# Kernel tuning notes

Hardware: AMD Instinct MI355X
Metric: run time of the kernel (lower is better)

The kernel has to match this reference:

```python
import jax, jax.numpy as jnp
import numpy as np

B, CIN, COUT, N, R, K = 8, 64, 64, 4096, 32, 3
LEAK = 0.2
BN_EPS = 1e-5
GN_EPS = 1e-5


def _voxelize(features, coords, r):
    # features: [B,C,N], coords: [B,3,N] -> grid [B,C,r,r,r], norm_coords [B,3,N]
    norm = coords - coords.mean(axis=2, keepdims=True)
    scale = jnp.max(jnp.linalg.norm(norm, axis=1, keepdims=True), axis=2, keepdims=True) * 2.0
    norm = norm / scale + 0.5
    norm = jnp.clip(norm * r, 0.0, r - 1.0)
    vox = jnp.round(norm).astype(jnp.int32)            # [B,3,N]
    idx = vox[:, 0] * (r * r) + vox[:, 1] * r + vox[:, 2]  # [B,N]
    b, c, n = features.shape
    r3 = r * r * r
    seg = (jnp.arange(b, dtype=jnp.int32)[:, None] * r3 + idx).reshape(-1)  # [B*N]
    feat = features.transpose(0, 2, 1).reshape(b * n, c)  # [B*N,C]
    sums = jax.ops.segment_sum(feat, seg, num_segments=b * r3)             # [B*r3,C]
    cnt = jax.ops.segment_sum(jnp.ones((b * n,), feat.dtype), seg, num_segments=b * r3)
    mean = sums / jnp.maximum(cnt, 1.0)[:, None]
    grid = mean.reshape(b, r3, c).transpose(0, 2, 1).reshape(b, c, r, r, r)
    return grid, norm


def _devoxelize(grid, norm_coords, r):
    # grid: [B,C,r,r,r], norm_coords: [B,3,N] in [0, r-1] -> [B,C,N]
    b, c = grid.shape[:2]
    flat = grid.reshape(b, c, r * r * r)
    cpos = jnp.clip(norm_coords, 0.0, r - 1.0)
    f = jnp.floor(cpos)
    d = cpos - f                                        # [B,3,N] frac
    i0 = f.astype(jnp.int32)
    i1 = jnp.minimum(i0 + 1, r - 1)
    out = jnp.zeros((b, c, norm_coords.shape[2]), grid.dtype)
    for dx in (0, 1):
        wx = d[:, 0] if dx else (1.0 - d[:, 0])
        ix = i1[:, 0] if dx else i0[:, 0]
        for dy in (0, 1):
            wy = d[:, 1] if dy else (1.0 - d[:, 1])
            iy = i1[:, 1] if dy else i0[:, 1]
            for dz in (0, 1):
                wz = d[:, 2] if dz else (1.0 - d[:, 2])
                iz = i1[:, 2] if dz else i0[:, 2]
                idx = ix * (r * r) + iy * r + iz        # [B,N]
                g = jnp.take_along_axis(flat, idx[:, None, :], axis=2)  # [B,C,N]
                out = out + (wx * wy * wz)[:, None, :] * g
    return out


def _conv3d(x, w, b):
    y = jax.lax.conv_general_dilated(x, w, window_strides=(1, 1, 1), padding='SAME',
                                     dimension_numbers=('NCDHW', 'OIDHW', 'NCDHW'))
    return y + b[None, :, None, None, None]


def _bn3d(x, g, bta, m, v):
    inv = g / jnp.sqrt(v + BN_EPS)
    return x * inv[None, :, None, None, None] + (bta - m * inv)[None, :, None, None, None]


def _leaky(x):
    return jnp.where(x >= 0, x, LEAK * x)


def _point_mlp(x, w, b, gg, gb):
    # Conv1d 1x1 + GroupNorm(8) + Swish; x: [B,Cin,N]
    y = jnp.einsum('oc,bcn->bon', w, x) + b[None, :, None]
    bb, cc, nn = y.shape
    yg = y.reshape(bb, 8, cc // 8, nn)
    mu = yg.mean(axis=(2, 3), keepdims=True)
    var = yg.var(axis=(2, 3), keepdims=True)
    yn = ((yg - mu) / jnp.sqrt(var + GN_EPS)).reshape(bb, cc, nn)
    yn = yn * gg[None, :, None] + gb[None, :, None]
    return yn * jax.nn.sigmoid(yn)  # Swish


def setup_inputs() -> dict:
    key = jax.random.key(0)
    ks = jax.random.split(key, 12)
    s3 = 1.0 / np.sqrt(CIN * K ** 3)
    s3b = 1.0 / np.sqrt(COUT * K ** 3)
    return {
        'features': jax.random.normal(ks[0], (B, CIN, N), jnp.float32),
        'coords': jax.random.normal(ks[1], (B, 3, N), jnp.float32),
        'temb': jax.random.normal(ks[2], (B, 64), jnp.float32),
        'conv1_w': jax.random.normal(ks[3], (COUT, CIN, K, K, K), jnp.float32) * s3,
        'conv1_b': jnp.zeros((COUT,), jnp.float32),
        'bn1_g': jnp.ones((COUT,), jnp.float32),
        'bn1_b': jnp.zeros((COUT,), jnp.float32),
        'bn1_m': jnp.zeros((COUT,), jnp.float32),
        'bn1_v': jnp.ones((COUT,), jnp.float32),
        'conv2_w': jax.random.normal(ks[4], (COUT, COUT, K, K, K), jnp.float32) * s3b,
        'conv2_b': jnp.zeros((COUT,), jnp.float32),
        'bn2_g': jnp.ones((COUT,), jnp.float32),
        'bn2_b': jnp.zeros((COUT,), jnp.float32),
        'bn2_m': jnp.zeros((COUT,), jnp.float32),
        'bn2_v': jnp.ones((COUT,), jnp.float32),
        'pf_w': jax.random.normal(ks[5], (COUT, CIN), jnp.float32) / np.sqrt(CIN),
        'pf_b': jnp.zeros((COUT,), jnp.float32),
        'gn_g': jnp.ones((COUT,), jnp.float32),
        'gn_b': jnp.zeros((COUT,), jnp.float32),
    }


def reference(features, coords, temb,
              conv1_w, conv1_b, bn1_g, bn1_b, bn1_m, bn1_v,
              conv2_w, conv2_b, bn2_g, bn2_b, bn2_m, bn2_v,
              pf_w, pf_b, gn_g, gn_b):
    grid, norm_coords = _voxelize(features, jax.lax.stop_gradient(coords), R)
    h = _leaky(_bn3d(_conv3d(grid, conv1_w, conv1_b), bn1_g, bn1_b, bn1_m, bn1_v))
    # dropout: identity in eval mode
    h = _leaky(_bn3d(_conv3d(h, conv2_w, conv2_b), bn2_g, bn2_b, bn2_m, bn2_v))
    vox_pts = _devoxelize(h, norm_coords, R)           # [B,COUT,N]
    fused = vox_pts + _point_mlp(features, pf_w, pf_b, gn_g, gn_b)
    return fused, coords, temb
```

## Files before the change

### kernel.cpp

```cpp
#include <hip/hip_runtime.h>
#include <hip/hip_bf16.h>
#include <math.h>

#define BB 8
#define CH 64
#define NP 4096
#define RG 32
#define R3 32768
#define LEAK 0.2f
#define BNEPS 1e-5f
#define GNEPS 1e-5f
#define SS3 602

typedef short short8 __attribute__((ext_vector_type(8)));
typedef float float4_ __attribute__((ext_vector_type(4)));

__device__ __forceinline__ short f2bf(float f){
  unsigned u = __float_as_uint(f);
  u += 0x7FFF + ((u>>16)&1);
  return (short)(u>>16);
}
__device__ __forceinline__ float bf2f(short s){
  unsigned u = ((unsigned)(unsigned short)s)<<16;
  return __uint_as_float(u);
}

__global__ void k_voxstats(const float* __restrict__ coords, float* __restrict__ ms){
  int b = blockIdx.x;
  __shared__ float red[256];
  float mean[3];
  for(int d=0; d<3; d++){
    float s=0.f;
    for(int i=threadIdx.x; i<NP; i+=256) s += coords[(b*3+d)*NP+i];
    red[threadIdx.x]=s; __syncthreads();
    for(int o=128;o>0;o>>=1){ if(threadIdx.x<o) red[threadIdx.x]+=red[threadIdx.x+o]; __syncthreads(); }
    mean[d]=red[0]/(float)NP; __syncthreads();
  }
  float mx=0.f;
  for(int i=threadIdx.x; i<NP; i+=256){
    float x=coords[(b*3+0)*NP+i]-mean[0];
    float y=coords[(b*3+1)*NP+i]-mean[1];
    float z=coords[(b*3+2)*NP+i]-mean[2];
    mx=fmaxf(mx, sqrtf(x*x+y*y+z*z));
  }
  red[threadIdx.x]=mx; __syncthreads();
  for(int o=128;o>0;o>>=1){ if(threadIdx.x<o) red[threadIdx.x]=fmaxf(red[threadIdx.x],red[threadIdx.x+o]); __syncthreads(); }
  if(threadIdx.x==0){
    ms[b*4+0]=mean[0]; ms[b*4+1]=mean[1]; ms[b*4+2]=mean[2];
    ms[b*4+3]=red[0]*2.0f;
  }
}

__global__ void k_assignzero(const float* __restrict__ coords, const float* __restrict__ ms,
                             float* __restrict__ nc, int* __restrict__ vi,
                             float* __restrict__ gsum){
  int bid=blockIdx.x;
  int blk=(bid&7)*1024 + (bid>>3);
  int wid = (blk*256+threadIdx.x)>>6;
  int lane = threadIdx.x&63;
  if(wid>=BB*NP) return;
  int b=wid>>12, n=wid&4095;
  float scale=ms[b*4+3];
  float v[3]; int vox[3];
  #pragma unroll
  for(int d=0; d<3; d++){
    float c=coords[(b*3+d)*NP+n] - ms[b*4+d];
    float vv=(c/scale + 0.5f)*32.0f;
    vv=fminf(fmaxf(vv,0.0f),31.0f);
    v[d]=vv;
    vox[d]=(int)rintf(vv);
  }
  int idx=vox[0]*1024+vox[1]*32+vox[2];
  if(lane<3) nc[(b*3+lane)*NP+n]=v[lane];
  if(lane==0) vi[wid]=idx;
  gsum[((size_t)b*R3+idx)*CH + lane]=0.f;
}

__global__ __launch_bounds__(256,2) void k_scatter(
    const float* __restrict__ feat, const int* __restrict__ vi,
    float* __restrict__ gsum, float* __restrict__ cnt){
  __shared__ float ft[64][65];
  int tid=threadIdx.x;
  int bid=blockIdx.x;
  int blk=(bid&7)*64 + (bid>>3);
  int b=blk>>6, n0=(blk&63)*64;
  for(int e=tid;e<4096;e+=256){
    int c=e>>6, nl=e&63;
    ft[nl][c]=feat[(size_t)(b*CH+c)*NP + n0+nl];
  }
  __syncthreads();
  int lane=tid&63, wv=tid>>6;
  for(int p=wv;p<64;p+=4){
    int idx=vi[(b<<12)+n0+p];
    atomicAdd(gsum + ((size_t)b*R3+idx)*CH + lane, ft[p][lane]);
    if(lane==0) atomicAdd(&cnt[b*R3+idx], 1.0f);
  }
}

__global__ void k_gridmean(const float* __restrict__ gsum, const float* __restrict__ cnt,
                           short* __restrict__ gbf){
  int bid=blockIdx.x;
  int blk=(bid&7)*1024 + (bid>>3);
  int t=blk*256+threadIdx.x;
  if(t>=BB*R3*8) return;
  int v=t>>3, q=t&7;
  float c=cnt[v];
  short8 o={0,0,0,0,0,0,0,0};
  if(c!=0.f){
    float inv=1.0f/c;
    const float* sp=gsum + (size_t)v*CH + q*8;
    #pragma unroll
    for(int j=0;j<8;j++) o[j]=f2bf(sp[j]*inv);
  }
  ((short8*)gbf)[(size_t)v*8+q]=o;
}

__global__ void k_wt3x2(const float* __restrict__ wa, const float* __restrict__ wb,
                        short* __restrict__ oa, short* __restrict__ ob){
  int t=blockIdx.x*256+threadIdx.x;
  if(t>=2*CH*CH*27) return;
  const float* w = (t<CH*CH*27)? wa : wb;
  short* o = (t<CH*CH*27)? oa : ob;
  int tt = (t<CH*CH*27)? t : t-CH*CH*27;
  int frag=tt>>9, l=(tt>>3)&63, j=tt&7;
  int tap=frag>>3, hh=(frag>>2)&1, nf=frag&3;
  int oc=nf*16+(l&15);
  int ci=hh*32+(l>>4)*8+j;
  o[tt]=f2bf(w[oc*1728 + ci*27 + tap]);
}

#define CONV_TAP(AF, BW) \
  _Pragma("unroll") for(int ks=0;ks<2;ks++) \
    _Pragma("unroll") for(int mf=0;mf<4;mf++) \
      _Pragma("unroll") for(int nf=0;nf<4;nf++) \
        acc[mf][nf]=__builtin_amdgcn_mfma_f32_16x16x32_bf16(AF[ks*4+mf],BW[ks*4+nf],acc[mf][nf],0,0,0);

__global__ __launch_bounds__(256,2) void k_conv_mfma(
    const short* __restrict__ gin, short* __restrict__ gout,
    const short* __restrict__ wt3, const float* __restrict__ bias,
    const float* __restrict__ bg, const float* __restrict__ bb,
    const float* __restrict__ bm, const float* __restrict__ bv){
  extern __shared__ __align__(16) short in_s[];
  int tid=threadIdx.x;
  int bid=blockIdx.x;
  int blk=(bid&7)*128 + (bid>>3);
  int b=blk>>7; int rem=blk&127;
  int zt=rem>>4, yt=(rem>>2)&3, xt=rem&3;
  int z0=zt*4, y0=yt*8, x0=xt*8;
  const short* gbase = gin + (size_t)b*R3*CH;

  int lane=tid&63, zl=tid>>6;
  int r15=lane&15, g=lane>>4;
  int ix=r15&7, iy=r15>>3;

  float4_ acc[4][4];
  #pragma unroll
  for(int mf=0;mf<4;mf++)
    #pragma unroll
    for(int nf=0;nf<4;nf++) acc[mf][nf]=(float4_){0.f,0.f,0.f,0.f};

  short8* s8=(short8*)in_s;

  for(int it=0; it<19; it++){
    int e=tid+it*256;
    if(e<4800){
      int ss=e>>3, cb=e&7;
      int z=ss/100, r2=ss-z*100, y=r2/10, x=r2-y*10;
      int gz=z0-1+z, gy=y0-1+y, gx=x0-1+x;
      short8 v={0,0,0,0,0,0,0,0};
      if(((unsigned)gz<32u)&&((unsigned)gy<32u)&&((unsigned)gx<32u))
        v=*(const short8*)(gbase + ((gz<<10)+(gy<<5)+gx)*CH + cb*8);
      s8[cb*SS3+ss]=v;
    }
  }
  __syncthreads();

  const short8* wb = ((const short8*)wt3) + lane;
  short8 bw0[8], bw1[8], aA[8], aB[8];
  #pragma unroll
  for(int f=0;f<8;f++) bw0[f]=wb[f*64];
  #pragma unroll
  for(int f=0;f<8;f++) bw1[f]=wb[512+f*64];
  #pragma unroll
  for(int ks=0;ks<2;ks++)
    #pragma unroll
    for(int mf=0;mf<4;mf++)
      aA[ks*4+mf]=s8[(ks*4+g)*SS3 + zl*100 + (mf*2+iy)*10 + ix];

  for(int tt=0; tt<27; tt+=2){
    if(tt+1<27){
      int t1=tt+1, kz=t1/9, r=t1-kz*9, ky=r/3, kx=r-ky*3;
      #pragma unroll
      for(int ks=0;ks<2;ks++)
        #pragma unroll
        for(int mf=0;mf<4;mf++)
          aB[ks*4+mf]=s8[(ks*4+g)*SS3 + (zl+kz)*100 + (mf*2+iy+ky)*10 + ix+kx];
    }
    CONV_TAP(aA, bw0);
    if(tt+2<27){
      #pragma unroll
      for(int f=0;f<8;f++) bw0[f]=wb[(tt+2)*512+f*64];
    }
    if(tt+1<27){
      if(tt+2<27){
        int t2=tt+2, kz=t2/9, r=t2-kz*9, ky=r/3, kx=r-ky*3;
        #pragma unroll
        for(int ks=0;ks<2;ks++)
          #pragma unroll
          for(int mf=0;mf<4;mf++)
            aA[ks*4+mf]=s8[(ks*4+g)*SS3 + (zl+kz)*100 + (mf*2+iy+ky)*10 + ix+kx];
      }
      CONV_TAP(aB, bw1);
      if(tt+3<27){
        #pragma unroll
        for(int f=0;f<8;f++) bw1[f]=wb[(tt+3)*512+f*64];
      }
    }
  }

  __syncthreads();
  short* ot=(short*)in_s;
  #pragma unroll
  for(int nf=0;nf<4;nf++){
    int oc=nf*16+r15;
    float iv=bg[oc]/sqrtf(bv[oc]+BNEPS);
    float sh=bias[oc]*iv + bb[oc]-bm[oc]*iv;
    #pragma unroll
    for(int mf=0;mf<4;mf++){
      #pragma unroll
      for(int q=0;q<4;q++){
        int m=mf*16+g*4+q;
        float val=acc[mf][nf][q]*iv+sh;
        val = val>=0.f ? val : LEAK*val;
        ot[(zl*64+m)*72 + oc]=f2bf(val);
      }
    }
  }
  __syncthreads();
  short* go = gout + (size_t)b*R3*CH;
  #pragma unroll
  for(int it=0;it<8;it++){
    int e=tid+it*256;
    int vr=e>>3, j=e&7;
    int zz=vr>>6, rr=vr&63;
    short8 v=*(short8*)(ot + vr*72 + j*8);
    *(short8*)(go + ((size_t)((z0+zz)*1024 + (y0+(rr>>3))*32 + x0+(rr&7)))*CH + j*8)=v;
  }
}

__global__ __launch_bounds__(256,2) void k_ptgemm(
    const float* __restrict__ feat, const float* __restrict__ w,
    const float* __restrict__ bias, float* __restrict__ y,
    float* __restrict__ stp){
  __shared__ float ws_[64*64];
  __shared__ float ft[64*64];
  __shared__ float sg[8], qg[8];
  int tid=threadIdx.x;
  int bid=blockIdx.x;
  int blk=(bid&7)*64 + (bid>>3);
  int b=blk>>6, n0=(blk&63)*64;
  for(int e=tid;e<4096;e+=256) ws_[e]=w[e];
  for(int e=tid;e<4096;e+=256){
    int c=e>>6, nl=e&63;
    ft[nl*64 + (c ^ ((nl&7)<<2))]=feat[(size_t)(b*CH+c)*NP + n0+nl];
  }
  if(tid<8){ sg[tid]=0.f; qg[tid]=0.f; }
  __syncthreads();
  int nl=tid&63, qq=tid>>6;
  float av[16];
  #pragma unroll
  for(int j=0;j<16;j++) av[j]=bias[qq*16+j];
  for(int c4=0;c4<64;c4+=4){
    float4_ fv=*(float4_*)&ft[nl*64 + (c4 ^ ((nl&7)<<2))];
    #pragma unroll
    for(int j=0;j<16;j++){
      float4_ wv4=*(float4_*)&ws_[(qq*16+j)*64+c4];
      av[j]=fmaf(fv[0],wv4[0],fmaf(fv[1],wv4[1],fmaf(fv[2],wv4[2],fmaf(fv[3],wv4[3],av[j]))));
    }
  }
  float* yp = y + ((size_t)(b*NP+n0+nl))*64 + qq*16;
  #pragma unroll
  for(int q4=0;q4<4;q4++)
    *(float4_*)(yp+q4*4)=(float4_){av[q4*4+0],av[q4*4+1],av[q4*4+2],av[q4*4+3]};
  float ps[2]={0.f,0.f}, pq[2]={0.f,0.f};
  #pragma unroll
  for(int j=0;j<16;j++){
    int gi=j>>3;
    ps[gi]+=av[j]; pq[gi]+=av[j]*av[j];
  }
  #pragma unroll
  for(int off=32;off>0;off>>=1){
    ps[0]+=__shfl_down(ps[0],off,64); pq[0]+=__shfl_down(pq[0],off,64);
    ps[1]+=__shfl_down(ps[1],off,64); pq[1]+=__shfl_down(pq[1],off,64);
  }
  if((tid&63)==0){
    atomicAdd(&sg[qq*2+0],ps[0]); atomicAdd(&qg[qq*2+0],pq[0]);
    atomicAdd(&sg[qq*2+1],ps[1]); atomicAdd(&qg[qq*2+1],pq[1]);
  }
  __syncthreads();
  if(tid<8){
    atomicAdd(&stp[(b*8+tid)*2+0], sg[tid]);
    atomicAdd(&stp[(b*8+tid)*2+1], qg[tid]);
  }
}

__global__ void k_fuse(const short* __restrict__ grid, const float* __restrict__ nc,
                       const float* __restrict__ py, const float* __restrict__ stp,
                       const float* __restrict__ gg, const float* __restrict__ gb,
                       float* __restrict__ out){
  __shared__ float ot[64][65];
  __shared__ float gmu[8], grs[8];
  int tid=threadIdx.x;
  int bid=blockIdx.x;
  int blk=(bid&7)*64 + (bid>>3);
  int b=blk>>6, n0=(blk&63)*64;
  int nl=tid>>2, qq=tid&3;
  int n=n0+nl;

  if(tid<8){
    float s=stp[(b*8+tid)*2+0], q=stp[(b*8+tid)*2+1];
    float mu=s/(8.f*NP);
    float var=q/(8.f*NP)-mu*mu;
    gmu[tid]=mu;
    grs[tid]=1.0f/sqrtf(var+GNEPS);
  }
  __syncthreads();

  float d_[3]; int i0[3], i1[3];
  #pragma unroll
  for(int dd=0;dd<3;dd++){
    float c=nc[(b*3+dd)*NP+n];
    c=fminf(fmaxf(c,0.f),31.f);
    float f=floorf(c);
    d_[dd]=c-f;
    i0[dd]=(int)f;
    i1[dd]=min(i0[dd]+1,31);
  }
  int idx8[8]; float w8[8];
  #pragma unroll
  for(int k=0;k<8;k++){
    int xx=(k&4)?i1[0]:i0[0];
    int yy=(k&2)?i1[1]:i0[1];
    int zz=(k&1)?i1[2]:i0[2];
    float wx=(k&4)?d_[0]:(1.f-d_[0]);
    float wy=(k&2)?d_[1]:(1.f-d_[1]);
    float wz=(k&1)?d_[2]:(1.f-d_[2]);
    idx8[k]=xx*1024+yy*32+zz;
    w8[k]=wx*wy*wz;
  }
  const short* gbase = grid + (size_t)b*R3*CH;
  const float* pp = py + ((size_t)(b*NP+n))*64;
  #pragma unroll
  for(int c8=0;c8<2;c8++){
    int c0=qq*16+c8*8;
    float dv[8]={0.f,0.f,0.f,0.f,0.f,0.f,0.f,0.f};
    #pragma unroll
    for(int k=0;k<8;k++){
      short8 gv=*(const short8*)(gbase + (size_t)idx8[k]*CH + c0);
      #pragma unroll
      for(int j=0;j<8;j++) dv[j]+=w8[k]*bf2f(gv[j]);
    }
    float4_ p0=*(const float4_*)(pp+c0);
    float4_ p1=*(const float4_*)(pp+c0+4);
    #pragma unroll
    for(int j=0;j<8;j++){
      int c=c0+j;
      float pv = j<4 ? p0[j] : p1[j-4];
      float yn=(pv-gmu[c>>3])*grs[c>>3]*gg[c]+gb[c];
      float sw=yn/(1.f+expf(-yn));
      ot[c][nl]=dv[j]+sw;
    }
  }
  __syncthreads();
  for(int i=tid;i<1024;i+=256){
    int c=i>>4, sg=i&15;
    float4_ v={ot[c][sg*4+0],ot[c][sg*4+1],ot[c][sg*4+2],ot[c][sg*4+3]};
    *(float4_*)(out + (size_t)(b*CH+c)*NP + n0 + sg*4) = v;
  }
}

__global__ void k_copyall(const float* __restrict__ coords, const float* __restrict__ temb,
                          float* __restrict__ out){
  int t=blockIdx.x*256+threadIdx.x;
  if(t<98304) out[2097152+t]=coords[t];
  else if(t<98816) out[2195456+(t-98304)]=temb[t-98304];
}

extern "C" void kernel_launch(void* const* d_in, const int* in_sizes, int n_in,
                              void* d_out, int out_size, void* d_ws, size_t ws_size,
                              hipStream_t stream){
  const float* features=(const float*)d_in[0];
  const float* coords  =(const float*)d_in[1];
  const float* temb    =(const float*)d_in[2];
  const float* c1w=(const float*)d_in[3];
  const float* c1b=(const float*)d_in[4];
  const float* b1g=(const float*)d_in[5];
  const float* b1b=(const float*)d_in[6];
  const float* b1m=(const float*)d_in[7];
  const float* b1v=(const float*)d_in[8];
  const float* c2w=(const float*)d_in[9];
  const float* c2b=(const float*)d_in[10];
  const float* b2g=(const float*)d_in[11];
  const float* b2b=(const float*)d_in[12];
  const float* b2m=(const float*)d_in[13];
  const float* b2v=(const float*)d_in[14];
  const float* pfw=(const float*)d_in[15];
  const float* pfb=(const float*)d_in[16];
  const float* gng=(const float*)d_in[17];
  const float* gnb=(const float*)d_in[18];

  float* F=(float*)d_ws;
  float* ms  = F + 0;
  float* nc  = F + 32;
  int*   vi  = (int*)(F + 98336);
  short* w1t = (short*)(F + 131104);
  short* w2t = (short*)(F + 186400);
  float* py  = F + 241696;
  float* stp = F + 2338848;
  float* cnt = F + 2338976;
  float* gA  = F + 2601120;
  short* gBF1= (short*)(F + 19378336);
  short* gBF2= (short*)(F + 27766944);
  float* out=(float*)d_out;

  static bool attr_set=false;
  if(!attr_set){
    hipFuncSetAttribute((const void*)k_conv_mfma,
                        hipFuncAttributeMaxDynamicSharedMemorySize, 77056);
    attr_set=true;
  }

  hipMemsetAsync(stp, 0, (size_t)(128+262144)*4, stream);

  k_voxstats <<<8,256,0,stream>>>(coords, ms);
  k_assignzero<<<8192,256,0,stream>>>(coords, ms, nc, vi, gA);
  k_scatter  <<<512,256,0,stream>>>(features, vi, gA, cnt);
  k_gridmean <<<8192,256,0,stream>>>(gA, cnt, gBF1);
  k_wt3x2    <<<864,256,0,stream>>>(c1w, c2w, w1t, w2t);
  k_conv_mfma<<<1024,256,77056,stream>>>(gBF1, gBF2, w1t, c1b, b1g, b1b, b1m, b1v);
  k_conv_mfma<<<1024,256,77056,stream>>>(gBF2, gBF1, w2t, c2b, b2g, b2b, b2m, b2v);
  k_ptgemm   <<<512,256,0,stream>>>(features, pfw, pfb, py, stp);
  k_fuse     <<<512,256,0,stream>>>(gBF1, nc, py, stp, gng, gnb, out);
  k_copyall  <<<386,256,0,stream>>>(coords, temb, out);
}
```

Baseline: 188.9 us.

## Split conv halo load into two stages, prefetching upper z-slices into registers during first taps

```diff
diff --git a/kernel.cpp b/kernel.cpp
--- a/kernel.cpp
+++ b/kernel.cpp
@@ -27,27 +27,34 @@
 
 __global__ void k_voxstats(const float* __restrict__ coords, float* __restrict__ ms){
   int b = blockIdx.x;
-  __shared__ float red[256];
-  float mean[3];
-  for(int d=0; d<3; d++){
-    float s=0.f;
-    for(int i=threadIdx.x; i<NP; i+=256) s += coords[(b*3+d)*NP+i];
-    red[threadIdx.x]=s; __syncthreads();
-    for(int o=128;o>0;o>>=1){ if(threadIdx.x<o) red[threadIdx.x]+=red[threadIdx.x+o]; __syncthreads(); }
-    mean[d]=red[0]/(float)NP; __syncthreads();
-  }
+  __shared__ float r0[256], r1[256], r2[256];
+  float s0=0.f, s1=0.f, s2=0.f;
+  const float* cx=coords+(size_t)(b*3+0)*NP;
+  const float* cy=coords+(size_t)(b*3+1)*NP;
+  const float* cz=coords+(size_t)(b*3+2)*NP;
+  for(int i=threadIdx.x; i<NP; i+=256){ s0+=cx[i]; s1+=cy[i]; s2+=cz[i]; }
+  r0[threadIdx.x]=s0; r1[threadIdx.x]=s1; r2[threadIdx.x]=s2;
+  __syncthreads();
+  for(int o=128;o>0;o>>=1){
+    if(threadIdx.x<o){
+      r0[threadIdx.x]+=r0[threadIdx.x+o];
+      r1[threadIdx.x]+=r1[threadIdx.x+o];
+      r2[threadIdx.x]+=r2[threadIdx.x+o];
+    }
+    __syncthreads();
+  }
+  float m0=r0[0]/(float)NP, m1=r1[0]/(float)NP, m2=r2[0]/(float)NP;
+  __syncthreads();
   float mx=0.f;
   for(int i=threadIdx.x; i<NP; i+=256){
-    float x=coords[(b*3+0)*NP+i]-mean[0];
-    float y=coords[(b*3+1)*NP+i]-mean[1];
-    float z=coords[(b*3+2)*NP+i]-mean[2];
+    float x=cx[i]-m0, y=cy[i]-m1, z=cz[i]-m2;
     mx=fmaxf(mx, sqrtf(x*x+y*y+z*z));
   }
-  red[threadIdx.x]=mx; __syncthreads();
-  for(int o=128;o>0;o>>=1){ if(threadIdx.x<o) red[threadIdx.x]=fmaxf(red[threadIdx.x],red[threadIdx.x+o]); __syncthreads(); }
+  r0[threadIdx.x]=mx; __syncthreads();
+  for(int o=128;o>0;o>>=1){ if(threadIdx.x<o) r0[threadIdx.x]=fmaxf(r0[threadIdx.x],r0[threadIdx.x+o]); __syncthreads(); }
   if(threadIdx.x==0){
-    ms[b*4+0]=mean[0]; ms[b*4+1]=mean[1]; ms[b*4+2]=mean[2];
-    ms[b*4+3]=red[0]*2.0f;
+    ms[b*4+0]=m0; ms[b*4+1]=m1; ms[b*4+2]=m2;
+    ms[b*4+3]=r0[0]*2.0f;
   }
 }
 
@@ -135,6 +142,32 @@
       _Pragma("unroll") for(int nf=0;nf<4;nf++) \
         acc[mf][nf]=__builtin_amdgcn_mfma_f32_16x16x32_bf16(AF[ks*4+mf],BW[ks*4+nf],acc[mf][nf],0,0,0);
 
+#define CONV_SEG(TT0, TT1) \
+  for(int tt=TT0; tt<TT1; tt+=2){ \
+    if(tt+1<TT1){ \
+      int t1=tt+1, kz=t1/9, r=t1-kz*9, ky=r/3, kx=r-ky*3; \
+      _Pragma("unroll") for(int ks=0;ks<2;ks++) \
+        _Pragma("unroll") for(int mf=0;mf<4;mf++) \
+          aB[ks*4+mf]=s8[(ks*4+g)*SS3 + (zl+kz)*100 + (mf*2+iy+ky)*10 + ix+kx]; \
+    } \
+    CONV_TAP(aA, bw0); \
+    if(tt+2<TT1){ \
+      _Pragma("unroll") for(int f=0;f<8;f++) bw0[f]=wb[(tt+2)*512+f*64]; \
+    } \
+    if(tt+1<TT1){ \
+      if(tt+2<TT1){ \
+        int t2=tt+2, kz=t2/9, r=t2-kz*9, ky=r/3, kx=r-ky*3; \
+        _Pragma("unroll") for(int ks=0;ks<2;ks++) \
+          _Pragma("unroll") for(int mf=0;mf<4;mf++) \
+            aA[ks*4+mf]=s8[(ks*4+g)*SS3 + (zl+kz)*100 + (mf*2+iy+ky)*10 + ix+kx]; \
+      } \
+      CONV_TAP(aB, bw1); \
+      if(tt+3<TT1){ \
+        _Pragma("unroll") for(int f=0;f<8;f++) bw1[f]=wb[(tt+3)*512+f*64]; \
+      } \
+    } \
+  }
+
 __global__ __launch_bounds__(256,2) void k_conv_mfma(
     const short* __restrict__ gin, short* __restrict__ gout,
     const short* __restrict__ wt3, const float* __restrict__ bias,
@@ -161,9 +194,9 @@
 
   short8* s8=(short8*)in_s;
 
-  for(int it=0; it<19; it++){
+  for(int it=0; it<13; it++){
     int e=tid+it*256;
-    if(e<4800){
+    if(e<3200){
       int ss=e>>3, cb=e&7;
       int z=ss/100, r2=ss-z*100, y=r2/10, x=r2-y*10;
       int gz=z0-1+z, gy=y0-1+y, gx=x0-1+x;
@@ -175,6 +208,21 @@
   }
   __syncthreads();
 
+  short8 pf[7];
+  #pragma unroll
+  for(int it=0; it<7; it++){
+    int u=tid+it*256;
+    short8 v={0,0,0,0,0,0,0,0};
+    if(u<1600){
+      int ss=400+(u>>3), cb=u&7;
+      int z=ss/100, r2=ss-z*100, y=r2/10, x=r2-y*10;
+      int gz=z0-1+z, gy=y0-1+y, gx=x0-1+x;
+      if(((unsigned)gz<32u)&&((unsigned)gy<32u)&&((unsigned)gx<32u))
+        v=*(const short8*)(gbase + ((gz<<10)+(gy<<5)+gx)*CH + cb*8);
+    }
+    pf[it]=v;
+  }
+
   const short8* wb = ((const short8*)wt3) + lane;
   short8 bw0[8], bw1[8], aA[8], aB[8];
   #pragma unroll
@@ -187,36 +235,29 @@
     for(int mf=0;mf<4;mf++)
       aA[ks*4+mf]=s8[(ks*4+g)*SS3 + zl*100 + (mf*2+iy)*10 + ix];
 
-  for(int tt=0; tt<27; tt+=2){
-    if(tt+1<27){
-      int t1=tt+1, kz=t1/9, r=t1-kz*9, ky=r/3, kx=r-ky*3;
-      #pragma unroll
-      for(int ks=0;ks<2;ks++)
-        #pragma unroll
-        for(int mf=0;mf<4;mf++)
-          aB[ks*4+mf]=s8[(ks*4+g)*SS3 + (zl+kz)*100 + (mf*2+iy+ky)*10 + ix+kx];
-    }
-    CONV_TAP(aA, bw0);
-    if(tt+2<27){
-      #pragma unroll
-      for(int f=0;f<8;f++) bw0[f]=wb[(tt+2)*512+f*64];
-    }
-    if(tt+1<27){
-      if(tt+2<27){
-        int t2=tt+2, kz=t2/9, r=t2-kz*9, ky=r/3, kx=r-ky*3;
-        #pragma unroll
-        for(int ks=0;ks<2;ks++)
-          #pragma unroll
-          for(int mf=0;mf<4;mf++)
-            aA[ks*4+mf]=s8[(ks*4+g)*SS3 + (zl+kz)*100 + (mf*2+iy+ky)*10 + ix+kx];
-      }
-      CONV_TAP(aB, bw1);
-      if(tt+3<27){
-        #pragma unroll
-        for(int f=0;f<8;f++) bw1[f]=wb[(tt+3)*512+f*64];
-      }
-    }
-  }
+  CONV_SEG(0, 9);
+
+  #pragma unroll
+  for(int it=0; it<7; it++){
+    int u=tid+it*256;
+    if(u<1600){
+      int ss=400+(u>>3), cb=u&7;
+      s8[cb*SS3+ss]=pf[it];
+    }
+  }
+  __syncthreads();
+
+  #pragma unroll
+  for(int f=0;f<8;f++) bw0[f]=wb[9*512+f*64];
+  #pragma unroll
+  for(int f=0;f<8;f++) bw1[f]=wb[10*512+f*64];
+  #pragma unroll
+  for(int ks=0;ks<2;ks++)
+    #pragma unroll
+    for(int mf=0;mf<4;mf++)
+      aA[ks*4+mf]=s8[(ks*4+g)*SS3 + (zl+1)*100 + (mf*2+iy)*10 + ix];
+
+  CONV_SEG(9, 27);
 
   __syncthreads();
   short* ot=(short*)in_s;
```

After: 180.7 us. -4.3%, faster.
